# Optimization experiments

Measured on AMD Instinct MI355X. Metric: run time of the kernel, lower is better.

Reference implementation:

```python
import jax, jax.numpy as jnp
import numpy as np

B, L, C, D = 8, 8192, 256, 256


def setup_inputs() -> dict:
    key = jax.random.key(0)
    ks = jax.random.split(key, 13)
    bound = 1.0 / np.sqrt(C)

    def W(k):
        return jax.random.uniform(k, (C, D), jnp.float32, -bound, bound)

    def b(k):
        return jax.random.uniform(k, (D,), jnp.float32, -bound, bound)

    return {
        "xs": jax.random.normal(ks[0], (B, L, C), jnp.float32),
        # forward-direction params
        "Wh1": W(ks[1]), "bh1": b(ks[2]),
        "Wz1": W(ks[3]), "bz1": b(ks[4]),
        "Ws1": W(ks[5]), "bs1": b(ks[6]),
        "h01": jnp.zeros((1, 1, D), jnp.float32),
        # backward-direction params
        "Wh_1": W(ks[7]), "bh_1": b(ks[8]),
        "Wz_1": W(ks[9]), "bz_1": b(ks[10]),
        "Ws_1": W(ks[11]), "bs_1": b(ks[12]),
        "h0_1": jnp.zeros((1, 1, D), jnp.float32),
    }


def _gru_scan(z, h_tilde, h0):
    """h[t] = z[t]*h_tilde[t] + (1-z[t])*h[t-1], h[-1]=h0. Parallel over time
    via associative scan on the affine maps h -> a*h + b."""
    a = 1.0 - z            # [B, L, D]
    b = z * h_tilde        # [B, L, D]

    def combine(c1, c2):
        a1, b1 = c1
        a2, b2 = c2
        return a1 * a2, a2 * b1 + b2

    A, Bc = jax.lax.associative_scan(combine, (a, b), axis=1)
    return Bc + A * h0     # broadcast h0 [1,1,D]


def reference(xs, Wh1, bh1, Wz1, bz1, Ws1, bs1, h01,
              Wh_1, bh_1, Wz_1, bz_1, Ws_1, bs_1, h0_1):
    sig = jax.nn.sigmoid
    # forward direction
    hf = _gru_scan(sig(xs @ Wz1 + bz1), xs @ Wh1 + bh1, h01) * sig(xs @ Ws1 + bs1)
    # backward direction: reverse time, scan, reverse back
    zr = sig(xs @ Wz_1 + bz_1)
    hr = xs @ Wh_1 + bh_1
    hb = _gru_scan(zr[:, ::-1], hr[:, ::-1], h0_1)[:, ::-1] * sig(xs @ Ws_1 + bs_1)
    return hf + hb
```

## Files before the change

### kernel.cpp

```cpp
#include <hip/hip_runtime.h>
#include <hip/hip_bf16.h>

typedef unsigned short u16;

#define BDIM 8
#define LDIM 8192
#define KDIM 256
#define DDIM 256
#define MTOT 65536
#define NDIM 1536
#define TCH  32
#define NCH  256


typedef float floatx4 __attribute__((ext_vector_type(4)));
typedef short bf16x8 __attribute__((ext_vector_type(8)));

__device__ __forceinline__ u16 f2bf(float f) {
  union { __hip_bfloat16 h; u16 u; } c;
  c.h = __float2bfloat16(f);
  return c.u;
}
__device__ __forceinline__ float bf2f(u16 u) {
  union { unsigned int i; float f; } c;
  c.i = ((unsigned int)u) << 16;
  return c.f;
}
__device__ __forceinline__ float sigmoidf_fast(float x) {
  return __builtin_amdgcn_rcpf(1.0f + __expf(-x));
}
__device__ __forceinline__ void gll16(const u16* g, u16* l) {
  __builtin_amdgcn_global_load_lds((const __attribute__((address_space(1))) void*)g,
                                   (__attribute__((address_space(3))) void*)l, 16, 0, 0);
}

__global__ void prep_weights(const float* __restrict__ Wh1, const float* __restrict__ Wz1,
                             const float* __restrict__ Ws1, const float* __restrict__ Wh_1,
                             const float* __restrict__ Wz_1, const float* __restrict__ Ws_1,
                             const float* __restrict__ bh1, const float* __restrict__ bz1,
                             const float* __restrict__ bs1, const float* __restrict__ bh_1,
                             const float* __restrict__ bz_1, const float* __restrict__ bs_1,
                             u16* __restrict__ WcatT, float* __restrict__ bcat) {
  const int n = blockIdx.x;
  const int k = threadIdx.x;
  const int nn = n & 63;
  const int p = (n & ~63) | ((nn & 15) << 2) | (nn >> 4);
  const int dir = p / 768, r = p % 768;
  int d; const float* W; const float* bb;
  if (r < 512) {
    d = r >> 1;
    if (r & 1) { W = dir ? Wz_1 : Wz1; bb = dir ? bz_1 : bz1; }
    else       { W = dir ? Wh_1 : Wh1; bb = dir ? bh_1 : bh1; }
  } else {
    d = r - 512;
    W = dir ? Ws_1 : Ws1; bb = dir ? bs_1 : bs1;
  }
  WcatT[(size_t)n * KDIM + k] = f2bf(W[k * DDIM + d]);
  if (k == 0) bcat[p] = bb[d];
}

__global__ __launch_bounds__(256) void gemm_kernel(const float* __restrict__ xs,
                                                   const u16* __restrict__ WcatT,
                                                   const float* __restrict__ bcat,
                                                   u16* __restrict__ G,
                                                   float* __restrict__ Acc,
                                                   float* __restrict__ Bcc) {
  __shared__ __align__(16) u16 sm[16384];
  u16* As = sm;
  u16* Bs = sm + 8192;
  const int tid = threadIdx.x;
  const int lane = tid & 63, wave = tid >> 6;
  const int wm = wave >> 1, wn = wave & 1;
  const int q = lane >> 4, r = lane & 15;

  const int xcd = blockIdx.x & 7;
  const int li  = blockIdx.x >> 3;
  const int mt  = xcd * 64 + li / 12;
  const int nt  = li % 12;
  const int m0 = mt * 128, n0 = nt * 128;

  const float* gAf[4]; const u16* gB[4]; u16* lA[4]; u16* lB[4];
#pragma unroll
  for (int j = 0; j < 4; j++) {
    const int bi = wave * 256 + j * 64 + lane;
    const int row = bi >> 3;
    const int kq = (bi & 7) ^ (row & 7);
    gAf[j] = xs    + (size_t)(m0 + row) * KDIM + kq * 8;
    gB[j]  = WcatT + (size_t)(n0 + row) * KDIM + kq * 8;
    lA[j] = As + bi * 8;
    lB[j] = Bs + bi * 8;
  }

  floatx4 acc[4][4];
  floatx4 z4 = {0.f, 0.f, 0.f, 0.f};
#pragma unroll
  for (int i = 0; i < 4; i++)
#pragma unroll
    for (int j = 0; j < 4; j++) acc[i][j] = z4;

  for (int k0 = 0; k0 < KDIM; k0 += 64) {
#pragma unroll
    for (int j = 0; j < 4; j++) gll16(gB[j] + k0, lB[j]);
#pragma unroll
    for (int j = 0; j < 4; j++) {
      const float4 f0 = *(const float4*)(gAf[j] + k0);
      const float4 f1 = *(const float4*)(gAf[j] + k0 + 4);
      union { u16 u[8]; uint4 v; } t;
      t.u[0] = f2bf(f0.x); t.u[1] = f2bf(f0.y); t.u[2] = f2bf(f0.z); t.u[3] = f2bf(f0.w);
      t.u[4] = f2bf(f1.x); t.u[5] = f2bf(f1.y); t.u[6] = f2bf(f1.z); t.u[7] = f2bf(f1.w);
      *(uint4*)lA[j] = t.v;
    }
    __syncthreads();
#pragma unroll
    for (int kk = 0; kk < 2; kk++) {
      bf16x8 af[4], bv[4];
#pragma unroll
      for (int i = 0; i < 4; i++) {
        const int row = wm * 64 + i * 16 + r;
        af[i] = *(const bf16x8*)(As + (row * 8 + ((kk * 4 + q) ^ (row & 7))) * 8);
      }
#pragma unroll
      for (int j = 0; j < 4; j++) {
        const int row = wn * 64 + j * 16 + r;
        bv[j] = *(const bf16x8*)(Bs + (row * 8 + ((kk * 4 + q) ^ (row & 7))) * 8);
      }
#pragma unroll
      for (int i = 0; i < 4; i++)
#pragma unroll
        for (int j = 0; j < 4; j++)
          acc[i][j] = __builtin_amdgcn_mfma_f32_16x16x32_bf16(af[i], bv[j], acc[i][j], 0, 0, 0);
    }
    __syncthreads();
  }

  const int pcol = wn * 64 + (r << 2);
  const float4 bv4 = *(const float4*)(bcat + n0 + pcol);
  const int hz = (n0 % 768) < 512;

  if (hz) {
#pragma unroll
    for (int i = 0; i < 4; i++) {
#pragma unroll
      for (int reg = 0; reg < 4; reg++) {
        const int lrow = wm * 64 + i * 16 + q * 4 + reg;
        union { u16 u[4]; uint2 v; } t;
        t.u[0] = f2bf(acc[i][0][reg] + bv4.x);
        t.u[1] = f2bf(acc[i][1][reg] + bv4.y);
        t.u[2] = f2bf(acc[i][2][reg] + bv4.z);
        t.u[3] = f2bf(acc[i][3][reg] + bv4.w);
        *(uint2*)(sm + lrow * 128 + pcol) = t.v;
      }
    }

    __syncthreads();

#pragma unroll
    for (int p = 0; p < 8; p++) {
      const int idx = p * 2048 + tid * 8;
      const int row = idx >> 7, col = idx & 127;
      const uint4 v = *(const uint4*)(sm + idx);
      *(uint4*)(G + (size_t)(m0 + row) * NDIM + n0 + col) = v;
    }

    const int cc = wave;
    const int dd = lane;
    const int dirn = n0 / 768;
    const int dbase = (n0 % 768) >> 1;
    const int bb = m0 >> 13;
    const int c0 = (m0 & 8191) >> 5;
    float h = 0.f, P = 1.f;
#pragma unroll 8
    for (int i = 0; i < TCH; ++i) {
      const int tl = dirn ? (TCH - 1 - i) : i;
      const unsigned int hzv = *(const unsigned int*)(sm + (cc * 32 + tl) * 128 + dd * 2);
      const float z = sigmoidf_fast(bf2f((u16)(hzv >> 16)));
      const float a = 1.f - z;
      h = fmaf(a, h, z * bf2f((u16)(hzv & 0xffffu)));
      P *= a;
    }
    const size_t u = (size_t)dirn * 2048 + (size_t)bb * 256 + (size_t)(c0 + cc);
    Acc[u * 256 + dbase + dd] = P;
    Bcc[u * 256 + dbase + dd] = h;
  } else {
#pragma unroll
    for (int i = 0; i < 4; i++) {
#pragma unroll
      for (int reg = 0; reg < 4; reg++) {
        const int lrow = wm * 64 + i * 16 + q * 4 + reg;
        union { u16 u[4]; uint2 v; } t;
        t.u[0] = f2bf(acc[i][0][reg] + bv4.x);
        t.u[1] = f2bf(acc[i][1][reg] + bv4.y);
        t.u[2] = f2bf(acc[i][2][reg] + bv4.z);
        t.u[3] = f2bf(acc[i][3][reg] + bv4.w);
        *(uint2*)(G + (size_t)(m0 + lrow) * NDIM + n0 + pcol) = t.v;
      }
    }
  }
}

__global__ void scan_phaseB(const float* __restrict__ Acc, const float* __restrict__ Bcc,
                            const float* __restrict__ h01, const float* __restrict__ h0_1,
                            float* __restrict__ Pref) {
  const int d = threadIdx.x, b = blockIdx.x, dir = blockIdx.y;
  float h = dir ? h0_1[d] : h01[d];
  const size_t ubase = ((size_t)dir * BDIM + b) * NCH;
  if (dir == 0) {
    for (int c0 = 0; c0 < NCH; c0 += 16) {
      float a[16], bb[16];
#pragma unroll
      for (int j = 0; j < 16; ++j) {
        size_t idx = (ubase + c0 + j) * DDIM + d;
        a[j] = Acc[idx]; bb[j] = Bcc[idx];
      }
#pragma unroll
      for (int j = 0; j < 16; ++j) {
        Pref[(ubase + c0 + j) * DDIM + d] = h;
        h = fmaf(a[j], h, bb[j]);
      }
    }
  } else {
    for (int c0 = NCH - 1; c0 >= 0; c0 -= 16) {
      float a[16], bb[16];
#pragma unroll
      for (int j = 0; j < 16; ++j) {
        size_t idx = (ubase + c0 - j) * DDIM + d;
        a[j] = Acc[idx]; bb[j] = Bcc[idx];
      }
#pragma unroll
      for (int j = 0; j < 16; ++j) {
        Pref[(ubase + c0 - j) * DDIM + d] = h;
        h = fmaf(a[j], h, bb[j]);
      }
    }
  }
}

__global__ __launch_bounds__(256) void scan_phaseC(const u16* __restrict__ G,
                                                   const float* __restrict__ Pref,
                                                   float* __restrict__ out) {
  __shared__ float obuf[TCH * 256];
  const int c = blockIdx.x & 255, b = blockIdx.x >> 8;
  const int dir = threadIdx.x >> 7;
  const int ld  = threadIdx.x & 127;
  const int d0 = ld * 2;
  const int u = dir * 2048 + b * 256 + c;
  const float2 h2 = *(const float2*)(Pref + (size_t)u * 256 + d0);
  float h0 = h2.x, h1 = h2.y;
  const u16* ghz = G + (size_t)b * LDIM * NDIM + dir * 768 + d0 * 2;
  const u16* gs  = G + (size_t)b * LDIM * NDIM + dir * 768 + 512 + d0;

#pragma unroll
  for (int i = 0; i < 16; ++i) {
    const int tl = dir ? (TCH - 1 - i) : i;
    const int t = c * TCH + tl;
    const uint2 hz4 = *(const uint2*)(ghz + (size_t)t * NDIM);
    const unsigned int s2 = *(const unsigned int*)(gs + (size_t)t * NDIM);
    const float z0 = sigmoidf_fast(bf2f((u16)(hz4.x >> 16)));
    const float z1 = sigmoidf_fast(bf2f((u16)(hz4.y >> 16)));
    h0 = fmaf(1.f - z0, h0, z0 * bf2f((u16)(hz4.x & 0xffffu)));
    h1 = fmaf(1.f - z1, h1, z1 * bf2f((u16)(hz4.y & 0xffffu)));
    float2 o;
    o.x = h0 * sigmoidf_fast(bf2f((u16)(s2 & 0xffffu)));
    o.y = h1 * sigmoidf_fast(bf2f((u16)(s2 >> 16)));
    *(float2*)(obuf + tl * 256 + d0) = o;
  }

  __syncthreads();

#pragma unroll
  for (int i = 16; i < 32; ++i) {
    const int tl = dir ? (TCH - 1 - i) : i;
    const int t = c * TCH + tl;
    const uint2 hz4 = *(const uint2*)(ghz + (size_t)t * NDIM);
    const unsigned int s2 = *(const unsigned int*)(gs + (size_t)t * NDIM);
    const float z0 = sigmoidf_fast(bf2f((u16)(hz4.x >> 16)));
    const float z1 = sigmoidf_fast(bf2f((u16)(hz4.y >> 16)));
    h0 = fmaf(1.f - z0, h0, z0 * bf2f((u16)(hz4.x & 0xffffu)));
    h1 = fmaf(1.f - z1, h1, z1 * bf2f((u16)(hz4.y & 0xffffu)));
    const float o0 = h0 * sigmoidf_fast(bf2f((u16)(s2 & 0xffffu)));
    const float o1 = h1 * sigmoidf_fast(bf2f((u16)(s2 >> 16)));
    const float2 other = *(const float2*)(obuf + tl * 256 + d0);
    float2 res;
    res.x = o0 + other.x;
    res.y = o1 + other.y;
    *(float2*)(out + ((size_t)b * LDIM + t) * DDIM + d0) = res;
  }
}

extern "C" void kernel_launch(void* const* d_in, const int* in_sizes, int n_in,
                              void* d_out, int out_size, void* d_ws, size_t ws_size,
                              hipStream_t stream) {
  const float* xs   = (const float*)d_in[0];
  const float* Wh1  = (const float*)d_in[1];
  const float* bh1  = (const float*)d_in[2];
  const float* Wz1  = (const float*)d_in[3];
  const float* bz1  = (const float*)d_in[4];
  const float* Ws1  = (const float*)d_in[5];
  const float* bs1  = (const float*)d_in[6];
  const float* h01  = (const float*)d_in[7];
  const float* Wh_1 = (const float*)d_in[8];
  const float* bh_1 = (const float*)d_in[9];
  const float* Wz_1 = (const float*)d_in[10];
  const float* bz_1 = (const float*)d_in[11];
  const float* Ws_1 = (const float*)d_in[12];
  const float* bs_1 = (const float*)d_in[13];
  const float* h0_1 = (const float*)d_in[14];
  float* out = (float*)d_out;

  char* ws = (char*)d_ws;
  u16* WcatT = (u16*)ws;   ws += (size_t)NDIM * KDIM * 2;
  float* bcat = (float*)ws; ws += (size_t)NDIM * 4;
  u16* G = (u16*)ws;       ws += (size_t)MTOT * NDIM * 2;

  const size_t sumElems = (size_t)2 * BDIM * NCH * DDIM;
  float* Acc  = (float*)ws; ws += sumElems * 4;
  float* Bcc  = (float*)ws; ws += sumElems * 4;
  float* Pref = (float*)ws; ws += sumElems * 4;
  if ((size_t)(ws - (char*)d_ws) > ws_size) return;

  prep_weights<<<dim3(NDIM), dim3(KDIM), 0, stream>>>(
      Wh1, Wz1, Ws1, Wh_1, Wz_1, Ws_1, bh1, bz1, bs1, bh_1, bz_1, bs_1, WcatT, bcat);
  gemm_kernel<<<dim3(6144), dim3(256), 0, stream>>>(xs, WcatT, bcat, G, Acc, Bcc);
  scan_phaseB<<<dim3(BDIM, 2), dim3(DDIM), 0, stream>>>(Acc, Bcc, h01, h0_1, Pref);
  scan_phaseC<<<dim3(2048), dim3(256), 0, stream>>>(G, Pref, out);
}
```

Measured before the change: 293.7 us.

## Pre-convert xs to bf16 once and use direct-to-LDS loads; nontemporal stores

Adds a conversion pass, fused into the weight-prep kernel, that writes xs as bf16 to a workspace buffer once. The GEMM then loads A tiles with global_load_lds like B, instead of each of the 12 N-tile blocks re-reading and converting fp32 xs in registers. G and the final output are written with nontemporal stores to reduce cache pollution. The trade-off is an extra read of xs (fp32) and write of 32 MB bf16 before the GEMM.

```diff
diff --git a/kernel.cpp b/kernel.cpp
--- a/kernel.cpp
+++ b/kernel.cpp
@@ -15,6 +15,9 @@
 
 typedef float floatx4 __attribute__((ext_vector_type(4)));
 typedef short bf16x8 __attribute__((ext_vector_type(8)));
+typedef unsigned int u32x4 __attribute__((ext_vector_type(4)));
+typedef unsigned int u32x2 __attribute__((ext_vector_type(2)));
+typedef float f32x2 __attribute__((ext_vector_type(2)));
 
 __device__ __forceinline__ u16 f2bf(float f) {
   union { __hip_bfloat16 h; u16 u; } c;
@@ -34,32 +37,47 @@
                                    (__attribute__((address_space(3))) void*)l, 16, 0, 0);
 }
 
-__global__ void prep_weights(const float* __restrict__ Wh1, const float* __restrict__ Wz1,
-                             const float* __restrict__ Ws1, const float* __restrict__ Wh_1,
-                             const float* __restrict__ Wz_1, const float* __restrict__ Ws_1,
-                             const float* __restrict__ bh1, const float* __restrict__ bz1,
-                             const float* __restrict__ bs1, const float* __restrict__ bh_1,
-                             const float* __restrict__ bz_1, const float* __restrict__ bs_1,
-                             u16* __restrict__ WcatT, float* __restrict__ bcat) {
-  const int n = blockIdx.x;
-  const int k = threadIdx.x;
-  const int nn = n & 63;
-  const int p = (n & ~63) | ((nn & 15) << 2) | (nn >> 4);
-  const int dir = p / 768, r = p % 768;
-  int d; const float* W; const float* bb;
-  if (r < 512) {
-    d = r >> 1;
-    if (r & 1) { W = dir ? Wz_1 : Wz1; bb = dir ? bz_1 : bz1; }
-    else       { W = dir ? Wh_1 : Wh1; bb = dir ? bh_1 : bh1; }
+__global__ void prep_conv(const float* __restrict__ Wh1, const float* __restrict__ Wz1,
+                          const float* __restrict__ Ws1, const float* __restrict__ Wh_1,
+                          const float* __restrict__ Wz_1, const float* __restrict__ Ws_1,
+                          const float* __restrict__ bh1, const float* __restrict__ bz1,
+                          const float* __restrict__ bs1, const float* __restrict__ bh_1,
+                          const float* __restrict__ bz_1, const float* __restrict__ bs_1,
+                          u16* __restrict__ WcatT, float* __restrict__ bcat,
+                          const float* __restrict__ xs, u16* __restrict__ Abf) {
+  if (blockIdx.x < NDIM) {
+    const int n = blockIdx.x;
+    const int k = threadIdx.x;
+    const int nn = n & 63;
+    const int p = (n & ~63) | ((nn & 15) << 2) | (nn >> 4);
+    const int dir = p / 768, r = p % 768;
+    int d; const float* W; const float* bb;
+    if (r < 512) {
+      d = r >> 1;
+      if (r & 1) { W = dir ? Wz_1 : Wz1; bb = dir ? bz_1 : bz1; }
+      else       { W = dir ? Wh_1 : Wh1; bb = dir ? bh_1 : bh1; }
+    } else {
+      d = r - 512;
+      W = dir ? Ws_1 : Ws1; bb = dir ? bs_1 : bs1;
+    }
+    WcatT[(size_t)n * KDIM + k] = f2bf(W[k * DDIM + d]);
+    if (k == 0) bcat[p] = bb[d];
   } else {
-    d = r - 512;
-    W = dir ? Ws_1 : Ws1; bb = dir ? bs_1 : bs1;
-  }
-  WcatT[(size_t)n * KDIM + k] = f2bf(W[k * DDIM + d]);
-  if (k == 0) bcat[p] = bb[d];
-}
-
-__global__ __launch_bounds__(256) void gemm_kernel(const float* __restrict__ xs,
+    const int cb = blockIdx.x - NDIM;
+#pragma unroll
+    for (int pass = 0; pass < 4; ++pass) {
+      size_t i = ((size_t)(pass * 2048 + cb) * 256 + threadIdx.x) * 8;
+      const float4* s = (const float4*)(xs + i);
+      float4 f0 = s[0], f1 = s[1];
+      union { u16 u[8]; u32x4 v; } t;
+      t.u[0] = f2bf(f0.x); t.u[1] = f2bf(f0.y); t.u[2] = f2bf(f0.z); t.u[3] = f2bf(f0.w);
+      t.u[4] = f2bf(f1.x); t.u[5] = f2bf(f1.y); t.u[6] = f2bf(f1.z); t.u[7] = f2bf(f1.w);
+      *(u32x4*)(Abf + i) = t.v;
+    }
+  }
+}
+
+__global__ __launch_bounds__(256) void gemm_kernel(const u16* __restrict__ Abf,
                                                    const u16* __restrict__ WcatT,
                                                    const float* __restrict__ bcat,
                                                    u16* __restrict__ G,
@@ -79,14 +97,14 @@
   const int nt  = li % 12;
   const int m0 = mt * 128, n0 = nt * 128;
 
-  const float* gAf[4]; const u16* gB[4]; u16* lA[4]; u16* lB[4];
+  const u16* gA[4]; const u16* gB[4]; u16* lA[4]; u16* lB[4];
 #pragma unroll
   for (int j = 0; j < 4; j++) {
     const int bi = wave * 256 + j * 64 + lane;
     const int row = bi >> 3;
     const int kq = (bi & 7) ^ (row & 7);
-    gAf[j] = xs    + (size_t)(m0 + row) * KDIM + kq * 8;
-    gB[j]  = WcatT + (size_t)(n0 + row) * KDIM + kq * 8;
+    gA[j] = Abf   + (size_t)(m0 + row) * KDIM + kq * 8;
+    gB[j] = WcatT + (size_t)(n0 + row) * KDIM + kq * 8;
     lA[j] = As + bi * 8;
     lB[j] = Bs + bi * 8;
   }
@@ -100,16 +118,7 @@
 
   for (int k0 = 0; k0 < KDIM; k0 += 64) {
 #pragma unroll
-    for (int j = 0; j < 4; j++) gll16(gB[j] + k0, lB[j]);
-#pragma unroll
-    for (int j = 0; j < 4; j++) {
-      const float4 f0 = *(const float4*)(gAf[j] + k0);
-      const float4 f1 = *(const float4*)(gAf[j] + k0 + 4);
-      union { u16 u[8]; uint4 v; } t;
-      t.u[0] = f2bf(f0.x); t.u[1] = f2bf(f0.y); t.u[2] = f2bf(f0.z); t.u[3] = f2bf(f0.w);
-      t.u[4] = f2bf(f1.x); t.u[5] = f2bf(f1.y); t.u[6] = f2bf(f1.z); t.u[7] = f2bf(f1.w);
-      *(uint4*)lA[j] = t.v;
-    }
+    for (int j = 0; j < 4; j++) { gll16(gA[j] + k0, lA[j]); gll16(gB[j] + k0, lB[j]); }
     __syncthreads();
 #pragma unroll
     for (int kk = 0; kk < 2; kk++) {
@@ -143,12 +152,12 @@
 #pragma unroll
       for (int reg = 0; reg < 4; reg++) {
         const int lrow = wm * 64 + i * 16 + q * 4 + reg;
-        union { u16 u[4]; uint2 v; } t;
+        union { u16 u[4]; u32x2 v; } t;
         t.u[0] = f2bf(acc[i][0][reg] + bv4.x);
         t.u[1] = f2bf(acc[i][1][reg] + bv4.y);
         t.u[2] = f2bf(acc[i][2][reg] + bv4.z);
         t.u[3] = f2bf(acc[i][3][reg] + bv4.w);
-        *(uint2*)(sm + lrow * 128 + pcol) = t.v;
+        *(u32x2*)(sm + lrow * 128 + pcol) = t.v;
       }
     }
 
@@ -158,8 +167,8 @@
     for (int p = 0; p < 8; p++) {
       const int idx = p * 2048 + tid * 8;
       const int row = idx >> 7, col = idx & 127;
-      const uint4 v = *(const uint4*)(sm + idx);
-      *(uint4*)(G + (size_t)(m0 + row) * NDIM + n0 + col) = v;
+      const u32x4 v = *(const u32x4*)(sm + idx);
+      __builtin_nontemporal_store(v, (u32x4*)(G + (size_t)(m0 + row) * NDIM + n0 + col));
     }
 
     const int cc = wave;
@@ -187,12 +196,12 @@
 #pragma unroll
       for (int reg = 0; reg < 4; reg++) {
         const int lrow = wm * 64 + i * 16 + q * 4 + reg;
-        union { u16 u[4]; uint2 v; } t;
+        union { u16 u[4]; u32x2 v; } t;
         t.u[0] = f2bf(acc[i][0][reg] + bv4.x);
         t.u[1] = f2bf(acc[i][1][reg] + bv4.y);
         t.u[2] = f2bf(acc[i][2][reg] + bv4.z);
         t.u[3] = f2bf(acc[i][3][reg] + bv4.w);
-        *(uint2*)(G + (size_t)(m0 + lrow) * NDIM + n0 + pcol) = t.v;
+        __builtin_nontemporal_store(t.v, (u32x2*)(G + (size_t)(m0 + lrow) * NDIM + n0 + pcol));
       }
     }
   }
@@ -280,10 +289,10 @@
     const float o0 = h0 * sigmoidf_fast(bf2f((u16)(s2 & 0xffffu)));
     const float o1 = h1 * sigmoidf_fast(bf2f((u16)(s2 >> 16)));
     const float2 other = *(const float2*)(obuf + tl * 256 + d0);
-    float2 res;
+    f32x2 res;
     res.x = o0 + other.x;
     res.y = o1 + other.y;
-    *(float2*)(out + ((size_t)b * LDIM + t) * DDIM + d0) = res;
+    __builtin_nontemporal_store(res, (f32x2*)(out + ((size_t)b * LDIM + t) * DDIM + d0));
   }
 }
 
@@ -310,6 +319,7 @@
   char* ws = (char*)d_ws;
   u16* WcatT = (u16*)ws;   ws += (size_t)NDIM * KDIM * 2;
   float* bcat = (float*)ws; ws += (size_t)NDIM * 4;
+  u16* Abf = (u16*)ws;     ws += (size_t)MTOT * KDIM * 2;
   u16* G = (u16*)ws;       ws += (size_t)MTOT * NDIM * 2;
 
   const size_t sumElems = (size_t)2 * BDIM * NCH * DDIM;
@@ -318,9 +328,10 @@
   float* Pref = (float*)ws; ws += sumElems * 4;
   if ((size_t)(ws - (char*)d_ws) > ws_size) return;
 
-  prep_weights<<<dim3(NDIM), dim3(KDIM), 0, stream>>>(
-      Wh1, Wz1, Ws1, Wh_1, Wz_1, Ws_1, bh1, bz1, bs1, bh_1, bz_1, bs_1, WcatT, bcat);
-  gemm_kernel<<<dim3(6144), dim3(256), 0, stream>>>(xs, WcatT, bcat, G, Acc, Bcc);
+  prep_conv<<<dim3(NDIM + 2048), dim3(256), 0, stream>>>(
+      Wh1, Wz1, Ws1, Wh_1, Wz_1, Ws_1, bh1, bz1, bs1, bh_1, bz_1, bs_1,
+      WcatT, bcat, xs, Abf);
+  gemm_kernel<<<dim3(6144), dim3(256), 0, stream>>>(Abf, WcatT, bcat, G, Acc, Bcc);
   scan_phaseB<<<dim3(BDIM, 2), dim3(DDIM), 0, stream>>>(Acc, Bcc, h01, h0_1, Pref);
   scan_phaseC<<<dim3(2048), dim3(256), 0, stream>>>(G, Pref, out);
 }
```

Measured after the change: 273.7 us. 1.07x faster.
